# Optimization experiments

Measured on AMD Instinct MI355X. Metric: run time of the kernel, lower is better.

Reference implementation:

```python
import jax, jax.numpy as jnp
import numpy as np

N_EMBD = 1024
N_HEAD = 16
HORIZON = 64
HS = N_EMBD // N_HEAD        # 64
BD = max(HS // 4, 16)        # 16


def setup_inputs() -> dict:
    key = jax.random.key(0)
    ks = jax.random.split(key, 12)
    s = 0.02
    B, T = 2, 1024
    return {
        "x": jax.random.normal(ks[0], (B, T, N_EMBD), jnp.float32),
        "W_disp": jax.random.normal(ks[1], (N_EMBD, N_HEAD * BD), jnp.float32) * s,
        "W_val": jax.random.normal(ks[2], (N_EMBD, N_EMBD), jnp.float32) * s,
        "rel_pos_emb": jax.random.normal(ks[3], (HORIZON, BD), jnp.float32) * s,
        "W_strain": jax.random.normal(ks[4], (BD, BD), jnp.float32) * s,
        "W_pos": jax.random.normal(ks[5], (BD, BD), jnp.float32) * s,
        "W_bond": jax.random.normal(ks[6], (BD, 1), jnp.float32) * s,
        "W_dmg": jax.random.normal(ks[7], (BD, BD), jnp.float32) * s,
        "b_dmg": jnp.zeros((BD,), jnp.float32),
        "W_dmg_out": jax.random.normal(ks[8], (BD, 1), jnp.float32) * s,
        "b_dmg_out": jnp.full((1,), -3.0, jnp.float32),  # nn.init.constant_(damage_out.bias, -3.0)
        "W_cproj": jax.random.normal(ks[9], (N_EMBD, N_EMBD), jnp.float32) * s,
    }


def _windows(t, delta):
    # t: (B, nh, T, D) -> (B, nh, T, delta, D); causal sliding window via left pad
    B, nh, T, D = t.shape
    padded = jnp.pad(t, ((0, 0), (0, 0), (delta - 1, 0), (0, 0)))
    idx = jnp.arange(T)[:, None] + jnp.arange(delta)[None, :]  # (T, delta)
    return padded[:, :, idx]  # gather over time axis


def reference(x, W_disp, W_val, rel_pos_emb, W_strain, W_pos, W_bond,
              W_dmg, b_dmg, W_dmg_out, b_dmg_out, W_cproj):
    B, T, C = x.shape
    nh, bd, hs = N_HEAD, BD, HS
    delta = min(HORIZON, T)

    disp = (x @ W_disp).reshape(B, T, nh, bd).transpose(0, 2, 1, 3)  # (B,nh,T,bd)
    val = (x @ W_val).reshape(B, T, nh, hs).transpose(0, 2, 1, 3)    # (B,nh,T,hs)

    disp_win = _windows(disp, delta)  # (B,nh,T,delta,bd)
    val_win = _windows(val, delta)    # (B,nh,T,delta,hs)

    # causal mask: window slot w for token t maps to position t - delta + 1 + w
    cmask = (jnp.arange(T)[:, None] - delta + 1 + jnp.arange(delta)[None, :]) >= 0  # (T,delta)

    strain = disp_win - disp[:, :, :, None, :]  # (B,nh,T,delta,bd)
    rel_emb = rel_pos_emb[:delta]               # (delta,bd)

    bond_act = jax.nn.gelu(strain @ W_strain + rel_emb @ W_pos, approximate=False)
    bond_logits = (bond_act @ W_bond)[..., 0]   # (B,nh,T,delta)

    damage_act = jax.nn.gelu(strain @ W_dmg + b_dmg, approximate=False)
    damage = jax.nn.sigmoid((damage_act @ W_dmg_out)[..., 0] + b_dmg_out[0])

    logits = bond_logits - 10.0 * damage
    logits = jnp.where(cmask[None, None], logits, -jnp.inf)
    weights = jax.nn.softmax(logits, axis=-1)

    out = jnp.einsum('bntd,bntde->bnte', weights, val_win)  # (B,nh,T,hs)
    out = out.transpose(0, 2, 1, 3).reshape(B, T, C)
    return out @ W_cproj
```

## Files before the change

kernel.cpp:

```cpp
#include <hip/hip_runtime.h>
#include <hip/hip_bf16.h>
#include <math.h>

#define TB   2
#define TT   1024
#define TC   1024
#define NH   16
#define HS   64
#define BDI  16
#define DLT  64
#define LDD  1280
#define GK   1024

typedef __attribute__((ext_vector_type(8))) short short8;
typedef __attribute__((ext_vector_type(4))) float floatx4;
typedef __hip_bfloat16 bf16;

__device__ __forceinline__ unsigned pkbf(float a, float b) {
    return (__float_as_uint(a) >> 16) | (__float_as_uint(b) & 0xFFFF0000u);
}

__device__ __forceinline__ float gelu_poly(float x) {
    float s = 0.5f * x * x;
    float q = fmaf(s, -1.f / 3.f, 1.f);
    return x * fmaf(0.3989422804f * x, q, 0.5f);
}

__device__ __forceinline__ void gload_lds16(const void* g, void* l) {
    __builtin_amdgcn_global_load_lds(
        (const __attribute__((address_space(1))) unsigned int*)(unsigned long long)g,
        (__attribute__((address_space(3))) unsigned int*)(unsigned int)(unsigned long long)l,
        16, 0, 0);
}

__device__ __forceinline__ void tpose_body(const float* __restrict__ in,
                                           bf16* __restrict__ outp,
                                           int k0, int n0, int N,
                                           float (*tile)[33], int tid) {
    const int tx = tid & 31, ty4 = (tid >> 5) * 4;
#pragma unroll
    for (int i = 0; i < 4; i++)
        tile[ty4 + i][tx] = in[(long long)(k0 + ty4 + i) * N + n0 + tx];
    __syncthreads();
#pragma unroll
    for (int i = 0; i < 4; i++)
        outp[(long long)(n0 + ty4 + i) * TC + k0 + tx] = __float2bfloat16(tile[tx][ty4 + i]);
}

__global__ __launch_bounds__(256) void prep_k(
    const float* __restrict__ x, const float* __restrict__ Wdisp,
    const float* __restrict__ Wval, const float* __restrict__ Wc,
    const float* __restrict__ rel, const float* __restrict__ Wp,
    bf16* __restrict__ xb, bf16* __restrict__ Wdvt, bf16* __restrict__ Wct,
    float* __restrict__ peG) {
    __shared__ float tile[32][33];
    const int blk = blockIdx.x, tid = threadIdx.x;
    if (blk < 2048) {
        int i = blk * 1024 + tid * 4;
        float4 v = *(const float4*)(x + i);
        bf16 o0 = __float2bfloat16(v.x), o1 = __float2bfloat16(v.y);
        bf16 o2 = __float2bfloat16(v.z), o3 = __float2bfloat16(v.w);
        ushort4 u;
        u.x = *(unsigned short*)&o0; u.y = *(unsigned short*)&o1;
        u.z = *(unsigned short*)&o2; u.w = *(unsigned short*)&o3;
        *(ushort4*)(xb + i) = u;
    } else if (blk < 2304) {
        int l = blk - 2048;
        tpose_body(Wdisp, Wdvt, (l >> 3) * 32, (l & 7) * 32, 256, tile, tid);
    } else if (blk < 3328) {
        int l = blk - 2304;
        tpose_body(Wval, Wdvt + (size_t)256 * TC, (l >> 5) * 32, (l & 31) * 32, TC, tile, tid);
    } else if (blk < 4352) {
        int l = blk - 3328;
        tpose_body(Wc, Wct, (l >> 5) * 32, (l & 31) * 32, TC, tile, tid);
    } else {
        int idx = (blk - 4352) * 256 + tid;
        int j = idx >> 4, d = idx & 15;
        float s = 0.f;
#pragma unroll
        for (int k = 0; k < BDI; k++)
            s += rel[j * BDI + k] * Wp[k * BDI + d];
        peG[idx] = s;
    }
}

template <int ID>
__global__ __launch_bounds__(256) void mfma_gemm_k(const bf16* __restrict__ A,
                                                   const bf16* __restrict__ Bt,
                                                   float* __restrict__ C,
                                                   int M, int N, int nbx) {
    __shared__ __align__(16) bf16 As[2][64 * 128];
    __shared__ __align__(16) bf16 Bs[2][64 * 128];
    const int tid = threadIdx.x;
    const int w = tid >> 6, lane = tid & 63;

    const int xcd = blockIdx.x & 7, s0 = blockIdx.x >> 3;
    const int l = xcd * (gridDim.x >> 3) + s0;
    const int row0 = (l / nbx) * 64, col0 = (l % nbx) * 64;
    const int wm = (w >> 1) * 32, wn = (w & 1) * 32;

    const bf16* gA[4];
    const bf16* gB[4];
    int lofs[4];
#pragma unroll
    for (int p = 0; p < 4; p++) {
        int u = (p * 4 + w) * 64 + lane;
        int r = u >> 4, s = u & 15;
        int c = s ^ (r & 15);
        gA[p] = A  + (long long)(row0 + r) * GK + c * 8;
        gB[p] = Bt + (long long)(col0 + r) * GK + c * 8;
        lofs[p] = (p * 4 + w) * 512;
    }

    floatx4 acc[2][2] = {};
    const int rA = lane & 15, quad = lane >> 4;

#pragma unroll
    for (int p = 0; p < 4; p++) {
        gload_lds16(gA[p], &As[0][lofs[p]]);
        gload_lds16(gB[p], &Bs[0][lofs[p]]);
    }

    int cur = 0;
    for (int k0 = 0; k0 < GK; k0 += 128) {
        __syncthreads();
        if (k0 + 128 < GK) {
#pragma unroll
            for (int p = 0; p < 4; p++) {
                gload_lds16(gA[p] + k0 + 128, &As[cur ^ 1][lofs[p]]);
                gload_lds16(gB[p] + k0 + 128, &Bs[cur ^ 1][lofs[p]]);
            }
        }
        const bf16* Ac = As[cur];
        const bf16* Bc = Bs[cur];
#pragma unroll
        for (int kh = 0; kh < 4; kh++) {
            const int g = kh * 4 + quad;
            short8 af[2], bfr[2];
#pragma unroll
            for (int i = 0; i < 2; i++) {
                af[i]  = *(const short8*)&Ac[(wm + i * 16 + rA) * 128 + ((g ^ rA) * 8)];
                bfr[i] = *(const short8*)&Bc[(wn + i * 16 + rA) * 128 + ((g ^ rA) * 8)];
            }
#pragma unroll
            for (int i = 0; i < 2; i++)
#pragma unroll
                for (int j = 0; j < 2; j++)
                    acc[i][j] = __builtin_amdgcn_mfma_f32_16x16x32_bf16(af[i], bfr[j], acc[i][j], 0, 0, 0);
        }
        cur ^= 1;
    }
    const int cn = lane & 15, rq = (lane >> 4) * 4;
#pragma unroll
    for (int i = 0; i < 2; i++)
#pragma unroll
        for (int j = 0; j < 2; j++) {
            long long base = (long long)(row0 + wm + i * 16 + rq) * N + col0 + wn + j * 16 + cn;
#pragma unroll
            for (int r = 0; r < 4; r++)
                C[base + (long long)r * N] = acc[i][j][r];
        }
}

__global__ __launch_bounds__(256) void attn_k(
    const float* __restrict__ dv,
    const float* __restrict__ peG,
    const float* __restrict__ W_strain,
    const float* __restrict__ W_dmg,
    const float* __restrict__ W_bond,
    const float* __restrict__ b_dmg,
    const float* __restrict__ W_dmg_out,
    const float* __restrict__ b_dmg_out,
    bf16* __restrict__ attnout) {
    __shared__ __align__(16) float sDisp[67][20];
    __shared__ __align__(16) float sVal[67][64];
    __shared__ float sWgt[4][DLT];

    const int tid = threadIdx.x;
    const int wave = tid >> 6;
    const int lane = tid & 63;
    const int xcd = blockIdx.x & 7, slot = blockIdx.x >> 3;
    const int bh = xcd * 4 + (slot >> 8);
    const int t0 = (slot & 255) * 4;
    const int h = bh & (NH - 1);
    const int b = bh >> 4;

    for (int idx = tid; idx < 67 * 4; idx += 256) {
        int r = idx >> 2, c = idx & 3;
        int row = t0 - 63 + r; row = row < 0 ? 0 : row;
        *(float4*)&sDisp[r][c * 4] =
            *(const float4*)(dv + (long long)(b * TT + row) * LDD + h * BDI + c * 4);
    }
    for (int idx = tid; idx < 67 * 16; idx += 256) {
        int r = idx >> 4, c = idx & 15;
        int row = t0 - 63 + r; row = row < 0 ? 0 : row;
        *(float4*)&sVal[r][c * 4] =
            *(const float4*)(dv + (long long)(b * TT + row) * LDD + 256 + h * HS + c * 4);
    }
    __syncthreads();

    const int t = t0 + wave;
    const int m = lane & 15, quad = lane >> 4;
    const short8 zero8 = {0, 0, 0, 0, 0, 0, 0, 0};
    union U8 { short8 s8; unsigned u[4]; };

    short8 bfs = zero8, bfd = zero8;
    if (quad < 2) {
        float ws[8], wd[8];
#pragma unroll
        for (int jj = 0; jj < 8; jj++) {
            int k = quad * 8 + jj;
            ws[jj] = W_strain[k * BDI + m];
            wd[jj] = W_dmg[k * BDI + m];
        }
        U8 a, c;
#pragma unroll
        for (int p = 0; p < 4; p++) {
            a.u[p] = pkbf(ws[2 * p], ws[2 * p + 1]);
            c.u[p] = pkbf(wd[2 * p], wd[2 * p + 1]);
        }
        bfs = a.s8; bfd = c.s8;
    }
    short8 af[4] = {zero8, zero8, zero8, zero8};
    if (quad < 2) {
        const float* op = &sDisp[wave + 63][quad * 8];
        float o[8];
        *(float4*)&o[0] = *(const float4*)op;
        *(float4*)&o[4] = *(const float4*)(op + 4);
#pragma unroll
        for (int q = 0; q < 4; q++) {
            const float* rp = &sDisp[wave + 16 * q + m][quad * 8];
            float p[8];
            *(float4*)&p[0] = *(const float4*)rp;
            *(float4*)&p[4] = *(const float4*)(rp + 4);
            U8 tpk;
#pragma unroll
            for (int pp = 0; pp < 4; pp++)
                tpk.u[pp] = pkbf(p[2 * pp] - o[2 * pp], p[2 * pp + 1] - o[2 * pp + 1]);
            af[q] = tpk.s8;
        }
    }

    const floatx4 zf = {0.f, 0.f, 0.f, 0.f};
    floatx4 cs[4], cd[4];
#pragma unroll
    for (int q = 0; q < 4; q++) {
        cs[q] = __builtin_amdgcn_mfma_f32_16x16x32_bf16(bfs, af[q], zf, 0, 0, 0);
        cd[q] = __builtin_amdgcn_mfma_f32_16x16x32_bf16(bfd, af[q], zf, 0, 0, 0);
    }

    const float4 wb4  = *(const float4*)(W_bond + 4 * quad);
    const float4 bd4  = *(const float4*)(b_dmg + 4 * quad);
    const float4 wdo4 = *(const float4*)(W_dmg_out + 4 * quad);
    float bq[4], dq[4];
#pragma unroll
    for (int q = 0; q < 4; q++) {
        const float4 pe4 = *(const float4*)(peG + (16 * q + m) * BDI + 4 * quad);
        float sb;
        sb = gelu_poly(cs[q][0] + pe4.x) * wb4.x;
        sb = fmaf(gelu_poly(cs[q][1] + pe4.y), wb4.y, sb);
        sb = fmaf(gelu_poly(cs[q][2] + pe4.z), wb4.z, sb);
        sb = fmaf(gelu_poly(cs[q][3] + pe4.w), wb4.w, sb);
        sb += __shfl_xor(sb, 16); sb += __shfl_xor(sb, 32);
        bq[q] = sb;
        float sd;
        sd = gelu_poly(cd[q][0] + bd4.x) * wdo4.x;
        sd = fmaf(gelu_poly(cd[q][1] + bd4.y), wdo4.y, sd);
        sd = fmaf(gelu_poly(cd[q][2] + bd4.z), wdo4.z, sd);
        sd = fmaf(gelu_poly(cd[q][3] + bd4.w), wdo4.w, sd);
        sd += __shfl_xor(sd, 16); sd += __shfl_xor(sd, 32);
        dq[q] = sd;
    }
    float bond = quad < 2 ? (quad == 0 ? bq[0] : bq[1])
                          : (quad == 2 ? bq[2] : bq[3]);
    float dmg  = quad < 2 ? (quad == 0 ? dq[0] : dq[1])
                          : (quad == 2 ? dq[2] : dq[3]);

    float damage = 1.f / (1.f + __expf(-(dmg + b_dmg_out[0])));
    const int tp0 = t - (DLT - 1);
    const bool valid = (tp0 + lane) >= 0;

    float e = valid ? __expf(bond - 10.f * damage) : 0.f;
    float sm = e;
#pragma unroll
    for (int off = 32; off >= 1; off >>= 1) sm += __shfl_xor(sm, off);
    float wgt = e / sm;

    sWgt[wave][lane] = wgt;
    float acc = 0.f;
#pragma unroll
    for (int g = 0; g < 16; g++) {
        float4 w4 = *(const float4*)&sWgt[wave][g * 4];
        acc = fmaf(w4.x, sVal[wave + g * 4 + 0][lane], acc);
        acc = fmaf(w4.y, sVal[wave + g * 4 + 1][lane], acc);
        acc = fmaf(w4.z, sVal[wave + g * 4 + 2][lane], acc);
        acc = fmaf(w4.w, sVal[wave + g * 4 + 3][lane], acc);
    }
    attnout[(long long)(b * TT + t) * TC + h * HS + lane] = __float2bfloat16(acc);
}

extern "C" void kernel_launch(void* const* d_in, const int* in_sizes, int n_in,
                              void* d_out, int out_size, void* d_ws, size_t ws_size,
                              hipStream_t stream) {
    const float* x      = (const float*)d_in[0];
    const float* W_disp = (const float*)d_in[1];
    const float* W_val  = (const float*)d_in[2];
    const float* rel    = (const float*)d_in[3];
    const float* Ws     = (const float*)d_in[4];
    const float* Wp     = (const float*)d_in[5];
    const float* Wb     = (const float*)d_in[6];
    const float* Wd     = (const float*)d_in[7];
    const float* bd_    = (const float*)d_in[8];
    const float* Wdo    = (const float*)d_in[9];
    const float* bdo    = (const float*)d_in[10];
    const float* Wc     = (const float*)d_in[11];
    float* out = (float*)d_out;

    const int M = TB * TT;
    char* ws = (char*)d_ws;
    bf16*  xb    = (bf16*)ws;
    bf16*  attnb = (bf16*)ws;
    bf16*  Wdvt  = (bf16*)(ws + (size_t)4 * 1024 * 1024);
    bf16*  Wct   = (bf16*)(ws + (size_t)6656 * 1024);
    float* dvC   = (float*)(ws + (size_t)8704 * 1024);
    float* peG   = (float*)(ws + (size_t)18944 * 1024);

    dim3 blk(256);
    prep_k<<<4356, blk, 0, stream>>>(x, W_disp, W_val, Wc, rel, Wp,
                                     xb, Wdvt, Wct, peG);
    mfma_gemm_k<1><<<(M / 64) * (LDD / 64), blk, 0, stream>>>(xb, Wdvt, dvC, M, LDD, LDD / 64);
    attn_k<<<(TB * NH * TT) / 4, blk, 0, stream>>>(dvC, peG, Ws, Wd, Wb, bd_,
                                                   Wdo, bdo, attnb);
    mfma_gemm_k<2><<<(M / 64) * (TC / 64), blk, 0, stream>>>(attnb, Wct, out, M, TC, TC / 64);
}
```

Measured before the change: 146.1 us.

## Process 16 tokens per attention block and use MFMA for weighted value sum

The attention kernel now handles 16 tokens per block instead of 4, with each wave looping over 4 tokens. This reuses the staged disp and value windows across more tokens, cutting redundant global loads. The weight-times-value reduction is recast as a bf16 MFMA over a banded weight matrix and a transposed bf16 value tile, replacing per-lane scalar FMAs. The gelu polynomial is also refactored to use fewer operations. Values and weights are now rounded to bf16 before the reduction, which adds some error.

After: 135.0 us. 1.08x faster.

```diff
diff --git a/kernel.cpp b/kernel.cpp
--- a/kernel.cpp
+++ b/kernel.cpp
@@ -20,10 +20,15 @@
     return (__float_as_uint(a) >> 16) | (__float_as_uint(b) & 0xFFFF0000u);
 }
 
+__device__ __forceinline__ unsigned bfbits(float x) {
+    bf16 h = __float2bfloat16(x);
+    return (unsigned)*(unsigned short*)&h;
+}
+
 __device__ __forceinline__ float gelu_poly(float x) {
-    float s = 0.5f * x * x;
-    float q = fmaf(s, -1.f / 3.f, 1.f);
-    return x * fmaf(0.3989422804f * x, q, 0.5f);
+    float y = x * x;
+    float p = fmaf(y, -0.06649038006f, 0.3989422804f);
+    return fmaf(x, 0.5f, y * p);
 }
 
 __device__ __forceinline__ void gload_lds16(const void* g, void* l) {
@@ -172,34 +177,46 @@
     const float* __restrict__ W_dmg_out,
     const float* __restrict__ b_dmg_out,
     bf16* __restrict__ attnout) {
-    __shared__ __align__(16) float sDisp[67][20];
-    __shared__ __align__(16) float sVal[67][64];
-    __shared__ float sWgt[4][DLT];
+    __shared__ __align__(16) float          sDisp[79][20];
+    __shared__ __align__(16) unsigned short sValT[64][104];
+    __shared__ __align__(16) unsigned short sWgtS[16][104];
 
     const int tid = threadIdx.x;
-    const int wave = tid >> 6;
-    const int lane = tid & 63;
+    const int wave = tid >> 6, lane = tid & 63;
     const int xcd = blockIdx.x & 7, slot = blockIdx.x >> 3;
-    const int bh = xcd * 4 + (slot >> 8);
-    const int t0 = (slot & 255) * 4;
+    const int bh = xcd * 4 + (slot >> 6);
+    const int t0 = (slot & 63) * 16;
     const int h = bh & (NH - 1);
     const int b = bh >> 4;
 
-    for (int idx = tid; idx < 67 * 4; idx += 256) {
+    if (tid < 208) ((int4*)sWgtS)[tid] = make_int4(0, 0, 0, 0);
+
+    for (int idx = tid; idx < 79 * 4; idx += 256) {
         int r = idx >> 2, c = idx & 3;
         int row = t0 - 63 + r; row = row < 0 ? 0 : row;
         *(float4*)&sDisp[r][c * 4] =
             *(const float4*)(dv + (long long)(b * TT + row) * LDD + h * BDI + c * 4);
     }
-    for (int idx = tid; idx < 67 * 16; idx += 256) {
-        int r = idx >> 4, c = idx & 15;
-        int row = t0 - 63 + r; row = row < 0 ? 0 : row;
-        *(float4*)&sVal[r][c * 4] =
-            *(const float4*)(dv + (long long)(b * TT + row) * LDD + 256 + h * HS + c * 4);
+    for (int idx = tid; idx < 24 * 16; idx += 256) {
+        int k4 = (idx >> 4) * 4, e4 = (idx & 15) * 4;
+        float vv[4][4];
+#pragma unroll
+        for (int rr = 0; rr < 4; rr++) {
+            int row = t0 - 63 + k4 + rr;
+            row = row < 0 ? 0 : (row > TT - 1 ? TT - 1 : row);
+            *(float4*)vv[rr] =
+                *(const float4*)(dv + (long long)(b * TT + row) * LDD + 256 + h * HS + e4);
+        }
+#pragma unroll
+        for (int e = 0; e < 4; e++) {
+            uint2 wv;
+            wv.x = bfbits(vv[0][e]) | (bfbits(vv[1][e]) << 16);
+            wv.y = bfbits(vv[2][e]) | (bfbits(vv[3][e]) << 16);
+            *(uint2*)&sValT[e4 + e][k4] = wv;
+        }
     }
     __syncthreads();
 
-    const int t = t0 + wave;
     const int m = lane & 15, quad = lane >> 4;
     const short8 zero8 = {0, 0, 0, 0, 0, 0, 0, 0};
     union U8 { short8 s8; unsigned u[4]; };
@@ -221,82 +238,91 @@
         }
         bfs = a.s8; bfd = c.s8;
     }
-    short8 af[4] = {zero8, zero8, zero8, zero8};
-    if (quad < 2) {
-        const float* op = &sDisp[wave + 63][quad * 8];
-        float o[8];
-        *(float4*)&o[0] = *(const float4*)op;
-        *(float4*)&o[4] = *(const float4*)(op + 4);
-#pragma unroll
-        for (int q = 0; q < 4; q++) {
-            const float* rp = &sDisp[wave + 16 * q + m][quad * 8];
-            float p[8];
-            *(float4*)&p[0] = *(const float4*)rp;
-            *(float4*)&p[4] = *(const float4*)(rp + 4);
-            U8 tpk;
-#pragma unroll
-            for (int pp = 0; pp < 4; pp++)
-                tpk.u[pp] = pkbf(p[2 * pp] - o[2 * pp], p[2 * pp + 1] - o[2 * pp + 1]);
-            af[q] = tpk.s8;
-        }
-    }
-
-    const floatx4 zf = {0.f, 0.f, 0.f, 0.f};
-    floatx4 cs[4], cd[4];
-#pragma unroll
-    for (int q = 0; q < 4; q++) {
-        cs[q] = __builtin_amdgcn_mfma_f32_16x16x32_bf16(bfs, af[q], zf, 0, 0, 0);
-        cd[q] = __builtin_amdgcn_mfma_f32_16x16x32_bf16(bfd, af[q], zf, 0, 0, 0);
-    }
-
     const float4 wb4  = *(const float4*)(W_bond + 4 * quad);
     const float4 bd4  = *(const float4*)(b_dmg + 4 * quad);
     const float4 wdo4 = *(const float4*)(W_dmg_out + 4 * quad);
-    float bq[4], dq[4];
-#pragma unroll
-    for (int q = 0; q < 4; q++) {
-        const float4 pe4 = *(const float4*)(peG + (16 * q + m) * BDI + 4 * quad);
-        float sb;
-        sb = gelu_poly(cs[q][0] + pe4.x) * wb4.x;
-        sb = fmaf(gelu_poly(cs[q][1] + pe4.y), wb4.y, sb);
-        sb = fmaf(gelu_poly(cs[q][2] + pe4.z), wb4.z, sb);
-        sb = fmaf(gelu_poly(cs[q][3] + pe4.w), wb4.w, sb);
-        sb += __shfl_xor(sb, 16); sb += __shfl_xor(sb, 32);
-        bq[q] = sb;
-        float sd;
-        sd = gelu_poly(cd[q][0] + bd4.x) * wdo4.x;
-        sd = fmaf(gelu_poly(cd[q][1] + bd4.y), wdo4.y, sd);
-        sd = fmaf(gelu_poly(cd[q][2] + bd4.z), wdo4.z, sd);
-        sd = fmaf(gelu_poly(cd[q][3] + bd4.w), wdo4.w, sd);
-        sd += __shfl_xor(sd, 16); sd += __shfl_xor(sd, 32);
-        dq[q] = sd;
-    }
-    float bond = quad < 2 ? (quad == 0 ? bq[0] : bq[1])
-                          : (quad == 2 ? bq[2] : bq[3]);
-    float dmg  = quad < 2 ? (quad == 0 ? dq[0] : dq[1])
-                          : (quad == 2 ? dq[2] : dq[3]);
-
-    float damage = 1.f / (1.f + __expf(-(dmg + b_dmg_out[0])));
-    const int tp0 = t - (DLT - 1);
-    const bool valid = (tp0 + lane) >= 0;
-
-    float e = valid ? __expf(bond - 10.f * damage) : 0.f;
-    float sm = e;
-#pragma unroll
-    for (int off = 32; off >= 1; off >>= 1) sm += __shfl_xor(sm, off);
-    float wgt = e / sm;
-
-    sWgt[wave][lane] = wgt;
-    float acc = 0.f;
-#pragma unroll
-    for (int g = 0; g < 16; g++) {
-        float4 w4 = *(const float4*)&sWgt[wave][g * 4];
-        acc = fmaf(w4.x, sVal[wave + g * 4 + 0][lane], acc);
-        acc = fmaf(w4.y, sVal[wave + g * 4 + 1][lane], acc);
-        acc = fmaf(w4.z, sVal[wave + g * 4 + 2][lane], acc);
-        acc = fmaf(w4.w, sVal[wave + g * 4 + 3][lane], acc);
-    }
-    attnout[(long long)(b * TT + t) * TC + h * HS + lane] = __float2bfloat16(acc);
+    const float bdo0  = b_dmg_out[0];
+    float4 pe4[4];
+#pragma unroll
+    for (int q = 0; q < 4; q++)
+        pe4[q] = *(const float4*)(peG + (16 * q + m) * BDI + 4 * quad);
+
+    const floatx4 zf = {0.f, 0.f, 0.f, 0.f};
+
+#pragma unroll
+    for (int s = 0; s < 4; s++) {
+        const int tau = 4 * wave + s;
+        short8 af[4] = {zero8, zero8, zero8, zero8};
+        if (quad < 2) {
+            const float* op = &sDisp[tau + 63][quad * 8];
+            float o[8];
+            *(float4*)&o[0] = *(const float4*)op;
+            *(float4*)&o[4] = *(const float4*)(op + 4);
+#pragma unroll
+            for (int q = 0; q < 4; q++) {
+                const float* rp = &sDisp[tau + 16 * q + m][quad * 8];
+                float p[8];
+                *(float4*)&p[0] = *(const float4*)rp;
+                *(float4*)&p[4] = *(const float4*)(rp + 4);
+                U8 tpk;
+#pragma unroll
+                for (int pp = 0; pp < 4; pp++)
+                    tpk.u[pp] = pkbf(p[2 * pp] - o[2 * pp], p[2 * pp + 1] - o[2 * pp + 1]);
+                af[q] = tpk.s8;
+            }
+        }
+        floatx4 cs[4], cd[4];
+#pragma unroll
+        for (int q = 0; q < 4; q++) {
+            cs[q] = __builtin_amdgcn_mfma_f32_16x16x32_bf16(bfs, af[q], zf, 0, 0, 0);
+            cd[q] = __builtin_amdgcn_mfma_f32_16x16x32_bf16(bfd, af[q], zf, 0, 0, 0);
+        }
+        float bq[4], dq[4];
+#pragma unroll
+        for (int q = 0; q < 4; q++) {
+            float sb;
+            sb = gelu_poly(cs[q][0] + pe4[q].x) * wb4.x;
+            sb = fmaf(gelu_poly(cs[q][1] + pe4[q].y), wb4.y, sb);
+            sb = fmaf(gelu_poly(cs[q][2] + pe4[q].z), wb4.z, sb);
+            sb = fmaf(gelu_poly(cs[q][3] + pe4[q].w), wb4.w, sb);
+            sb += __shfl_xor(sb, 16); sb += __shfl_xor(sb, 32);
+            bq[q] = sb;
+            float sd;
+            sd = gelu_poly(cd[q][0] + bd4.x) * wdo4.x;
+            sd = fmaf(gelu_poly(cd[q][1] + bd4.y), wdo4.y, sd);
+            sd = fmaf(gelu_poly(cd[q][2] + bd4.z), wdo4.z, sd);
+            sd = fmaf(gelu_poly(cd[q][3] + bd4.w), wdo4.w, sd);
+            sd += __shfl_xor(sd, 16); sd += __shfl_xor(sd, 32);
+            dq[q] = sd;
+        }
+        float bond = quad < 2 ? (quad == 0 ? bq[0] : bq[1])
+                              : (quad == 2 ? bq[2] : bq[3]);
+        float dmg  = quad < 2 ? (quad == 0 ? dq[0] : dq[1])
+                              : (quad == 2 ? dq[2] : dq[3]);
+
+        float damage = 1.f / (1.f + __expf(-(dmg + bdo0)));
+        const bool valid = (t0 + tau - 63 + lane) >= 0;
+        float e = valid ? __expf(bond - 10.f * damage) : 0.f;
+        float sm = e;
+#pragma unroll
+        for (int off = 32; off >= 1; off >>= 1) sm += __shfl_xor(sm, off);
+        sWgtS[tau][tau + lane] = (unsigned short)bfbits(e / sm);
+    }
+    __syncthreads();
+
+    floatx4 acc = zf;
+#pragma unroll
+    for (int c = 0; c < 3; c++) {
+        short8 afr = *(const short8*)&sWgtS[m][c * 32 + quad * 8];
+        short8 bfr = *(const short8*)&sValT[16 * wave + m][c * 32 + quad * 8];
+        acc = __builtin_amdgcn_mfma_f32_16x16x32_bf16(afr, bfr, acc, 0, 0, 0);
+    }
+    const int e0 = 16 * wave + m;
+#pragma unroll
+    for (int r = 0; r < 4; r++) {
+        int tau = quad * 4 + r;
+        attnout[(long long)(b * TT + t0 + tau) * TC + h * HS + e0] = __float2bfloat16(acc[r]);
+    }
 }
 
 extern "C" void kernel_launch(void* const* d_in, const int* in_sizes, int n_in,
@@ -329,7 +355,7 @@
     prep_k<<<4356, blk, 0, stream>>>(x, W_disp, W_val, Wc, rel, Wp,
                                      xb, Wdvt, Wct, peG);
     mfma_gemm_k<1><<<(M / 64) * (LDD / 64), blk, 0, stream>>>(xb, Wdvt, dvC, M, LDD, LDD / 64);
-    attn_k<<<(TB * NH * TT) / 4, blk, 0, stream>>>(dvC, peG, Ws, Wd, Wb, bd_,
-                                                   Wdo, bdo, attnb);
+    attn_k<<<(TB * NH * TT) / 16, blk, 0, stream>>>(dvC, peG, Ws, Wd, Wb, bd_,
+                                                    Wdo, bdo, attnb);
     mfma_gemm_k<2><<<(M / 64) * (TC / 64), blk, 0, stream>>>(attnb, Wct, out, M, TC, TC / 64);
 }
```
